# Optimization experiments

Measured on AMD Instinct MI355X. Metric: run time of the kernel, lower is better.

The kernel has to match this reference:

```python
import jax, jax.numpy as jnp
import numpy as np

HEADS = 8
DIM_HEAD = 64


def setup_inputs() -> dict:
    key = jax.random.key(0)
    ks = jax.random.split(key, 6)
    b, dim, h, w = 8, 512, 64, 64
    inner = HEADS * DIM_HEAD  # 512
    return {
        "f_m": jax.random.normal(ks[0], (b, dim, h, w), dtype=jnp.float32),
        "f_n": jax.random.normal(ks[1], (b, dim, h, w), dtype=jnp.float32),
        "Wq": jax.random.normal(ks[2], (inner, dim), dtype=jnp.float32) * 0.02,
        "Wkv": jax.random.normal(ks[3], (2 * inner, dim), dtype=jnp.float32) * 0.02,
        "Wout": jax.random.normal(ks[4], (dim, inner), dtype=jnp.float32) * 0.02,
        "bout": jax.random.normal(ks[5], (dim,), dtype=jnp.float32) * 0.02,
    }


def reference(f_m, f_n, Wq, Wkv, Wout, bout):
    b, c, h, w = f_m.shape
    n = h * w
    scale = DIM_HEAD ** -0.5
    # 1x1 convs == channel GEMMs
    q = jnp.einsum('oc,bchw->bohw', Wq, f_m).reshape(b, HEADS, DIM_HEAD, n)
    kv = jnp.einsum('oc,bchw->bohw', Wkv, f_n)
    k, v = jnp.split(kv, 2, axis=1)
    k = k.reshape(b, HEADS, DIM_HEAD, n)
    v = v.reshape(b, HEADS, DIM_HEAD, n)
    # NOTE: contraction is over spatial n -> channel attention [b,h,d,d]
    dots = jnp.einsum('bhin,bhjn->bhij', q, k) * scale
    attn = jax.nn.softmax(dots, axis=-1)
    out = jnp.einsum('bhij,bhjn->bhin', attn, v).reshape(b, HEADS * DIM_HEAD, h, w)
    return jnp.einsum('oc,bchw->bohw', Wout, out) + bout[None, :, None, None]
```

## Files before the change

### kernel.cpp

```cpp
#include <hip/hip_runtime.h>
#include <hip/hip_bf16.h>
#include <stdint.h>

typedef __bf16 bf16_t;
typedef __bf16 bf16x8 __attribute__((ext_vector_type(8)));
typedef float f32x4 __attribute__((ext_vector_type(4)));

#define MFMA_16x16x32(A, B, C) __builtin_amdgcn_mfma_f32_16x16x32_bf16((A), (B), (C), 0, 0, 0)

__device__ inline void gload_lds16(const bf16_t* g, bf16_t* lds) {
  auto* gp = (const __attribute__((address_space(1))) uint32_t*)(uintptr_t)g;
  auto* lp = (__attribute__((address_space(3))) uint32_t*)(uintptr_t)lds;
  __builtin_amdgcn_global_load_lds(gp, lp, 16, 0, 0);
}

__global__ __launch_bounds__(256)
void k_cvt3(const float* __restrict__ a, const float* __restrict__ b,
            const float* __restrict__ c, bf16_t* __restrict__ oa,
            bf16_t* __restrict__ ob, bf16_t* __restrict__ oc) {
  int i = blockIdx.x * blockDim.x + threadIdx.x;
  int region = i >> 16;
  int e = (i & 65535) * 4;
  const float* src = region == 0 ? a : (region == 1 ? b : c);
  bf16_t* dst = region == 0 ? oa : (region == 1 ? ob : oc);
  float4 v = *(const float4*)(src + e);
  bf16_t o[4] = {(bf16_t)v.x, (bf16_t)v.y, (bf16_t)v.z, (bf16_t)v.w};
  *(uint2*)(dst + e) = *(uint2*)o;
}

__global__ __launch_bounds__(256)
void k_transpose_cast(const float* __restrict__ in, bf16_t* __restrict__ out, int C, int N) {
  __shared__ float tile[32][33];
  int b = blockIdx.z;
  const float* src = in + (size_t)b * C * N;
  bf16_t* dst = out + (size_t)b * C * N;
  int n0 = blockIdx.x * 32, c0 = blockIdx.y * 32;
  int tx = threadIdx.x, ty = threadIdx.y;
#pragma unroll
  for (int i = 0; i < 32; i += 8)
    tile[ty + i][tx] = src[(size_t)(c0 + ty + i) * N + (n0 + tx)];
  __syncthreads();
#pragma unroll
  for (int i = 0; i < 32; i += 8)
    dst[(size_t)(n0 + ty + i) * C + (c0 + tx)] = (bf16_t)tile[tx][ty + i];
}

__global__ __launch_bounds__(256)
void k_fnT(const float* __restrict__ in, bf16_t* __restrict__ out_nc, int C, int N) {
  __shared__ float tile[64][65];
  const int b = blockIdx.z;
  const float* src = in + (size_t)b * C * N;
  const int n0 = blockIdx.x * 64, c0 = blockIdx.y * 64;
  const int t = threadIdx.x;
  const int cr = t >> 2;
  const int nc = (t & 3) * 16;
  {
    const float* srow = src + (size_t)(c0 + cr) * N + n0 + nc;
#pragma unroll
    for (int q = 0; q < 4; ++q) {
      float4 v = *(const float4*)(srow + q * 4);
      tile[cr][nc + q * 4 + 0] = v.x; tile[cr][nc + q * 4 + 1] = v.y;
      tile[cr][nc + q * 4 + 2] = v.z; tile[cr][nc + q * 4 + 3] = v.w;
    }
  }
  __syncthreads();
  {
    const int nr = t >> 2;
    const int cc = (t & 3) * 16;
    bf16_t on[16];
#pragma unroll
    for (int q = 0; q < 16; ++q) on[q] = (bf16_t)tile[cc + q][nr];
    bf16_t* dst = out_nc + (size_t)b * (size_t)N * C + (size_t)(n0 + nr) * C + c0 + cc;
    *(uint4*)(dst) = *(uint4*)(on);
    *(uint4*)(dst + 8) = *(uint4*)(on + 8);
  }
}

__global__ __launch_bounds__(512, 2)
void k_gram256(const float* __restrict__ A, const float* __restrict__ B,
               bf16_t* __restrict__ Cp) {
  const int raw = blockIdx.x;
  const int xcd = raw & 7, idx = raw >> 3;
  const int mt = idx & 1, nt = (idx >> 1) & 1, ks = idx >> 2;
  const int b = xcd;
  const float* Ab = A + (size_t)b * 512 * 4096;
  const float* Bb = B + (size_t)b * 512 * 4096;
  const int bm = mt * 256, bn = nt * 256;
  const int kbeg = ks * 512;

  const int tid = threadIdx.x;
  const int wave = tid >> 6, lane = tid & 63;
  const int l15 = lane & 15, l4 = lane >> 4;
  const int wm = (wave >> 2) * 128, wn = (wave & 3) * 64;
  const int rsw = (l15 >> 1) & 3;

  __shared__ bf16_t As[2][256 * 32];
  __shared__ bf16_t Bs[2][256 * 32];

  f32x4 acc[8][4] = {};

  const int rho = tid >> 1, h = tid & 1;
  const int sw = (rho >> 1) & 3;
  const int wo0 = rho * 32 + (((2 * h) ^ sw) * 8);
  const int wo1 = rho * 32 + (((2 * h + 1) ^ sw) * 8);
  const float* ga = Ab + (size_t)(bm + rho) * 4096 + kbeg + h * 16;
  const float* gb = Bb + (size_t)(bn + rho) * 4096 + kbeg + h * 16;

  float4 ra[4], rb[4];
#pragma unroll
  for (int q = 0; q < 4; ++q) {
    ra[q] = *(const float4*)(ga + q * 4);
    rb[q] = *(const float4*)(gb + q * 4);
  }

  int cur = 0;
  for (int i = 0; i < 16; ++i) {
    bf16_t ta[16], tb[16];
#pragma unroll
    for (int q = 0; q < 4; ++q) {
      ta[q * 4 + 0] = (bf16_t)ra[q].x; ta[q * 4 + 1] = (bf16_t)ra[q].y;
      ta[q * 4 + 2] = (bf16_t)ra[q].z; ta[q * 4 + 3] = (bf16_t)ra[q].w;
      tb[q * 4 + 0] = (bf16_t)rb[q].x; tb[q * 4 + 1] = (bf16_t)rb[q].y;
      tb[q * 4 + 2] = (bf16_t)rb[q].z; tb[q * 4 + 3] = (bf16_t)rb[q].w;
    }
    *(uint4*)(&As[cur][wo0]) = *(uint4*)(ta);
    *(uint4*)(&As[cur][wo1]) = *(uint4*)(ta + 8);
    *(uint4*)(&Bs[cur][wo0]) = *(uint4*)(tb);
    *(uint4*)(&Bs[cur][wo1]) = *(uint4*)(tb + 8);
    if (i + 1 < 16) {
      const float* na = ga + (i + 1) * 32;
      const float* nb = gb + (i + 1) * 32;
#pragma unroll
      for (int q = 0; q < 4; ++q) {
        ra[q] = *(const float4*)(na + q * 4);
        rb[q] = *(const float4*)(nb + q * 4);
      }
    }
    __syncthreads();
    bf16x8 bfr[4];
#pragma unroll
    for (int n = 0; n < 4; ++n)
      bfr[n] = *(const bf16x8*)(&Bs[cur][(wn + n * 16 + l15) * 32 + ((l4 ^ rsw) * 8)]);
#pragma unroll
    for (int m = 0; m < 8; ++m) {
      bf16x8 af = *(const bf16x8*)(&As[cur][(wm + m * 16 + l15) * 32 + ((l4 ^ rsw) * 8)]);
#pragma unroll
      for (int n = 0; n < 4; ++n)
        acc[m][n] = MFMA_16x16x32(af, bfr[n], acc[m][n]);
    }
    cur ^= 1;
  }

  bf16_t* Cb = Cp + (size_t)(b * 8 + ks) * 262144;
#pragma unroll
  for (int m = 0; m < 8; ++m) {
    const int row0 = bm + wm + m * 16 + l4 * 4;
#pragma unroll
    for (int n = 0; n < 4; ++n) {
      const int col = bn + wn + n * 16 + l15;
#pragma unroll
      for (int j = 0; j < 4; ++j)
        Cb[(size_t)(row0 + j) * 512 + col] = (bf16_t)acc[m][n][j];
    }
  }
}

__global__ __launch_bounds__(512, 2)
void k_y256(const bf16_t* __restrict__ A, const bf16_t* __restrict__ B,
            float* __restrict__ C, const float* __restrict__ bias) {
  const int raw = blockIdx.x;
  const int b = raw & 7, c = raw >> 3;
  const int bm = (c & 1) * 256, bn = (c >> 1) * 256;
  A += (size_t)b * 262144;
  B += (size_t)b * 4096 * 512;
  C += (size_t)b * 512 * 4096;

  const int tid = threadIdx.x;
  const int wave = tid >> 6, lane = tid & 63;
  const int l15 = lane & 15, l4 = lane >> 4;
  const int wm = (wave >> 2) * 128, wn = (wave & 3) * 64;
  const int rsw = (l15 >> 1) & 3;

  __shared__ bf16_t As[2][256 * 32];
  __shared__ bf16_t Bs[2][256 * 32];

  f32x4 acc[8][4] = {};

  const int lrow = lane >> 2;
  const int lch = (lane & 3) ^ ((lane >> 3) & 3);
  const bf16_t* srcA = A + (size_t)(bm + wave * 32 + lrow) * 512 + lch * 8;
  const bf16_t* srcB = B + (size_t)(bn + wave * 32 + lrow) * 512 + lch * 8;
  bf16_t* dstA = &As[0][wave * 32 * 32];
  bf16_t* dstB = &Bs[0][wave * 32 * 32];
  const int bufoff = 256 * 32;

  auto stage = [&](int buf, int k0) {
    gload_lds16(srcA + k0,            dstA + buf * bufoff);
    gload_lds16(srcA + 16 * 512 + k0, dstA + buf * bufoff + 512);
    gload_lds16(srcB + k0,            dstB + buf * bufoff);
    gload_lds16(srcB + 16 * 512 + k0, dstB + buf * bufoff + 512);
  };

  stage(0, 0);
  __syncthreads();

  int cur = 0;
  for (int i = 0; i < 16; ++i) {
    if (i + 1 < 16) stage(cur ^ 1, (i + 1) * 32);
    bf16x8 bfr[4];
#pragma unroll
    for (int n = 0; n < 4; ++n)
      bfr[n] = *(const bf16x8*)(&Bs[cur][(wn + n * 16 + l15) * 32 + ((l4 ^ rsw) * 8)]);
#pragma unroll
    for (int m = 0; m < 8; ++m) {
      bf16x8 af = *(const bf16x8*)(&As[cur][(wm + m * 16 + l15) * 32 + ((l4 ^ rsw) * 8)]);
#pragma unroll
      for (int n = 0; n < 4; ++n)
        acc[m][n] = MFMA_16x16x32(af, bfr[n], acc[m][n]);
    }
    __syncthreads();
    cur ^= 1;
  }

#pragma unroll
  for (int m = 0; m < 8; ++m) {
    const int row0 = bm + wm + m * 16 + l4 * 4;
#pragma unroll
    for (int n = 0; n < 4; ++n) {
      const int col = bn + wn + n * 16 + l15;
#pragma unroll
      for (int j = 0; j < 4; ++j)
        C[(size_t)(row0 + j) * 4096 + col] = acc[m][n][j] + bias[row0 + j];
    }
  }
}

__global__ __launch_bounds__(256)
void k_reduce8(const bf16_t* __restrict__ p, bf16_t* __restrict__ out) {
  int i = blockIdx.x * blockDim.x + threadIdx.x;
  int b = i >> 15;
  int e8 = (i & 32767) * 8;
  const bf16_t* pb = p + (size_t)b * 8 * 262144 + e8;
  float s[8] = {};
#pragma unroll
  for (int ks = 0; ks < 8; ++ks) {
    bf16x8 v = *(const bf16x8*)(pb + (size_t)ks * 262144);
#pragma unroll
    for (int j = 0; j < 8; ++j) s[j] += (float)v[j];
  }
  bf16x8 o;
#pragma unroll
  for (int j = 0; j < 8; ++j) o[j] = (bf16_t)s[j];
  *(bf16x8*)(out + (size_t)b * 262144 + e8) = o;
}

__global__ __launch_bounds__(256)
void k_gemm_bt(const bf16_t* __restrict__ A, const bf16_t* __restrict__ B,
               bf16_t* __restrict__ Cv, int M, int N, int K,
               long long sA, long long sB, long long sC) {
  const int zb = blockIdx.z;
  A += (size_t)zb * sA;
  B += (size_t)zb * sB;

  const int tid = threadIdx.x;
  const int wave = tid >> 6, lane = tid & 63;
  const int l15 = lane & 15, l4 = lane >> 4;
  const int bm = blockIdx.y * 128, bn = blockIdx.x * 128;
  const int wm = (wave >> 1) * 64, wn = (wave & 1) * 64;

  __shared__ bf16_t As[2][128 * 32];
  __shared__ bf16_t Bs[2][128 * 32];

  f32x4 acc[4][4] = {};

  const int lrow = lane >> 2;
  const int lchunk = (lane & 3) * 8;
  const int ra = wave * 16 + lrow;

  auto stage = [&](int buf, int k0) {
    gload_lds16(&A[(size_t)(bm + ra) * K + k0 + lchunk],      &As[buf][(wave * 16) * 32]);
    gload_lds16(&A[(size_t)(bm + 64 + ra) * K + k0 + lchunk], &As[buf][(64 + wave * 16) * 32]);
    gload_lds16(&B[(size_t)(bn + ra) * K + k0 + lchunk],      &Bs[buf][(wave * 16) * 32]);
    gload_lds16(&B[(size_t)(bn + 64 + ra) * K + k0 + lchunk], &Bs[buf][(64 + wave * 16) * 32]);
  };

  const int nsteps = K / 32;
  stage(0, 0);
  __syncthreads();

  for (int i = 0; i < nsteps; ++i) {
    const int cur = i & 1;
    if (i + 1 < nsteps) stage(cur ^ 1, (i + 1) * 32);
    bf16x8 af[4], bfr[4];
#pragma unroll
    for (int m = 0; m < 4; ++m)
      af[m] = *(const bf16x8*)(&As[cur][(wm + m * 16 + l15) * 32 + l4 * 8]);
#pragma unroll
    for (int n = 0; n < 4; ++n)
      bfr[n] = *(const bf16x8*)(&Bs[cur][(wn + n * 16 + l15) * 32 + l4 * 8]);
#pragma unroll
    for (int m = 0; m < 4; ++m)
#pragma unroll
      for (int n = 0; n < 4; ++n)
        acc[m][n] = MFMA_16x16x32(af[m], bfr[n], acc[m][n]);
    __syncthreads();
  }

#pragma unroll
  for (int m = 0; m < 4; ++m) {
    const int row0 = bm + wm + m * 16 + l4 * 4;
#pragma unroll
    for (int n = 0; n < 4; ++n) {
      const int col = bn + wn + n * 16 + l15;
#pragma unroll
      for (int j = 0; j < 4; ++j)
        (Cv + (size_t)zb * sC)[(size_t)(row0 + j) * N + col] = (bf16_t)acc[m][n][j];
    }
  }
}

__global__ __launch_bounds__(256)
void k_dots_wveff(const bf16_t* __restrict__ T1, const bf16_t* __restrict__ wk,
                  const bf16_t* __restrict__ wvT, bf16_t* __restrict__ wveffT) {
  const int bh = blockIdx.x;
  const int b = bh >> 3, hh = bh & 7;
  const bf16_t* qh = T1 + (size_t)b * 262144 + (size_t)hh * 64 * 512;
  const bf16_t* kh = wk + (size_t)hh * 64 * 512;
  const int tid = threadIdx.x;
  const int wave = tid >> 6, lane = tid & 63;
  const int l15 = lane & 15, l4 = lane >> 4;

  __shared__ float S[64][65];
  __shared__ bf16_t P[64][72];

  {
    const int wm = (wave >> 1) * 32, wn = (wave & 1) * 32;
    f32x4 acc[2][2] = {};
#pragma unroll 2
    for (int k0 = 0; k0 < 512; k0 += 32) {
      bf16x8 af[2], bfr[2];
#pragma unroll
      for (int m = 0; m < 2; ++m)
        af[m] = *(const bf16x8*)(&qh[(size_t)(wm + m * 16 + l15) * 512 + k0 + l4 * 8]);
#pragma unroll
      for (int n = 0; n < 2; ++n)
        bfr[n] = *(const bf16x8*)(&kh[(size_t)(wn + n * 16 + l15) * 512 + k0 + l4 * 8]);
#pragma unroll
      for (int m = 0; m < 2; ++m)
#pragma unroll
        for (int n = 0; n < 2; ++n)
          acc[m][n] = MFMA_16x16x32(af[m], bfr[n], acc[m][n]);
    }
    const float scale = 0.125f;
#pragma unroll
    for (int m = 0; m < 2; ++m)
#pragma unroll
      for (int n = 0; n < 2; ++n)
#pragma unroll
        for (int j = 0; j < 4; ++j)
          S[wm + m * 16 + l4 * 4 + j][wn + n * 16 + l15] = acc[m][n][j] * scale;
  }
  __syncthreads();

  {
    const int r = tid >> 2, seg = (tid & 3) * 16;
    float vals[16];
    float mx = -1e30f;
#pragma unroll
    for (int c = 0; c < 16; ++c) { vals[c] = S[r][seg + c]; mx = fmaxf(mx, vals[c]); }
    mx = fmaxf(mx, __shfl_xor(mx, 1));
    mx = fmaxf(mx, __shfl_xor(mx, 2));
    float sum = 0.f;
#pragma unroll
    for (int c = 0; c < 16; ++c) { vals[c] = __expf(vals[c] - mx); sum += vals[c]; }
    sum += __shfl_xor(sum, 1);
    sum += __shfl_xor(sum, 2);
    const float inv = 1.0f / sum;
    bf16_t pr[16];
#pragma unroll
    for (int c = 0; c < 16; ++c) pr[c] = (bf16_t)(vals[c] * inv);
    *(uint4*)(&P[r][seg]) = *(uint4*)(pr);
    *(uint4*)(&P[r][seg + 8]) = *(uint4*)(pr + 8);
  }
  __syncthreads();

  {
    const bf16_t* av = wvT + (size_t)hh * 512 * 64;
    bf16_t* ob = wveffT + (size_t)b * 262144 + (size_t)hh * 64;
    const int wm = (wave >> 1) * 64, wn = (wave & 1) * 32;
    for (int cm0 = 0; cm0 < 512; cm0 += 128) {
      f32x4 acc[4][2] = {};
#pragma unroll
      for (int ks = 0; ks < 2; ++ks) {
        const int k0 = ks * 32;
        bf16x8 af[4], bfr[2];
#pragma unroll
        for (int m = 0; m < 4; ++m)
          af[m] = *(const bf16x8*)(&av[(size_t)(cm0 + wm + m * 16 + l15) * 64 + k0 + l4 * 8]);
#pragma unroll
        for (int n = 0; n < 2; ++n)
          bfr[n] = *(const bf16x8*)(&P[wn + n * 16 + l15][k0 + l4 * 8]);
#pragma unroll
        for (int m = 0; m < 4; ++m)
#pragma unroll
          for (int n = 0; n < 2; ++n)
            acc[m][n] = MFMA_16x16x32(af[m], bfr[n], acc[m][n]);
      }
#pragma unroll
      for (int m = 0; m < 4; ++m)
#pragma unroll
        for (int n = 0; n < 2; ++n)
#pragma unroll
          for (int j = 0; j < 4; ++j)
            ob[(size_t)(cm0 + wm + m * 16 + l4 * 4 + j) * 512 + wn + n * 16 + l15] =
                (bf16_t)acc[m][n][j];
    }
  }
}

extern "C" void kernel_launch(void* const* d_in, const int* in_sizes, int n_in,
                              void* d_out, int out_size, void* d_ws, size_t ws_size,
                              hipStream_t stream) {
  const float* f_m  = (const float*)d_in[0];
  const float* f_n  = (const float*)d_in[1];
  const float* Wq   = (const float*)d_in[2];
  const float* Wkv  = (const float*)d_in[3];
  const float* Wout = (const float*)d_in[4];
  const float* bout = (const float*)d_in[5];
  float* y = (float*)d_out;

  const size_t ACT = (size_t)8 * 4096 * 512;
  const size_t SQ  = (size_t)512 * 512;
  char* p = (char*)d_ws;
  bf16_t* wq_b    = (bf16_t*)p; p += SQ * 2;
  bf16_t* wk_b    = (bf16_t*)p; p += SQ * 2;
  bf16_t* wout_b  = (bf16_t*)p; p += SQ * 2;
  bf16_t* wvT     = (bf16_t*)p; p += SQ * 2;
  bf16_t* Hb      = (bf16_t*)p; p += (size_t)8 * SQ * 2;
  bf16_t* T1      = (bf16_t*)p; p += (size_t)8 * SQ * 2;
  bf16_t* wveffT  = (bf16_t*)p; p += (size_t)8 * SQ * 2;
  bf16_t* W2      = (bf16_t*)p; p += (size_t)8 * SQ * 2;
  bf16_t* Hp8     = (bf16_t*)p; p += (size_t)64 * SQ * 2;
  bf16_t* fnT     = (bf16_t*)p; p += ACT * 2;

  k_cvt3<<<dim3(768), 256, 0, stream>>>(Wq, Wkv, Wout, wq_b, wk_b, wout_b);
  k_transpose_cast<<<dim3(16, 2, 8), dim3(32, 8), 0, stream>>>(Wkv + SQ, wvT, 64, 512);

  k_fnT<<<dim3(64, 8, 8), 256, 0, stream>>>(f_n, fnT, 512, 4096);

  k_gram256<<<dim3(256), 512, 0, stream>>>(f_n, f_m, Hp8);
  k_reduce8<<<dim3(1024), 256, 0, stream>>>(Hp8, Hb);

  k_gemm_bt<<<dim3(4, 4, 8), 256, 0, stream>>>(wq_b, Hb, T1, 512, 512, 512,
                                               0, (long long)SQ, (long long)SQ);
  k_dots_wveff<<<dim3(64), 256, 0, stream>>>(T1, wk_b, wvT, wveffT);
  k_gemm_bt<<<dim3(4, 4, 8), 256, 0, stream>>>(wout_b, wveffT, W2, 512, 512, 512,
                                               0, (long long)SQ, (long long)SQ);
  k_y256<<<dim3(256), 512, 0, stream>>>(W2, fnT, y, bout);
}
```

Baseline: 135.7 us.

## Merge front-end prep kernels and gram GEMM into one heterogeneous launch

Combines the weight cast, Wv transpose, f_n transpose-cast and the partial Gram GEMM into a single kernel whose blocks dispatch on block index to the different jobs. This removes three launches and lets the memory-bound transpose and cast blocks run alongside the compute-bound gram blocks. In exchange, every block reserves 64KB of LDS and uses 512 threads, so the small transpose and cast blocks may have lower occupancy. The ordering of block scheduling now decides how well the two kinds of work overlap.

```diff
diff --git a/kernel.cpp b/kernel.cpp
--- a/kernel.cpp
+++ b/kernel.cpp
@@ -14,224 +14,161 @@
   __builtin_amdgcn_global_load_lds(gp, lp, 16, 0, 0);
 }
 
-__global__ __launch_bounds__(256)
-void k_cvt3(const float* __restrict__ a, const float* __restrict__ b,
-            const float* __restrict__ c, bf16_t* __restrict__ oa,
-            bf16_t* __restrict__ ob, bf16_t* __restrict__ oc) {
-  int i = blockIdx.x * blockDim.x + threadIdx.x;
-  int region = i >> 16;
-  int e = (i & 65535) * 4;
-  const float* src = region == 0 ? a : (region == 1 ? b : c);
-  bf16_t* dst = region == 0 ? oa : (region == 1 ? ob : oc);
-  float4 v = *(const float4*)(src + e);
-  bf16_t o[4] = {(bf16_t)v.x, (bf16_t)v.y, (bf16_t)v.z, (bf16_t)v.w};
-  *(uint2*)(dst + e) = *(uint2*)o;
-}
-
-__global__ __launch_bounds__(256)
-void k_transpose_cast(const float* __restrict__ in, bf16_t* __restrict__ out, int C, int N) {
-  __shared__ float tile[32][33];
-  int b = blockIdx.z;
-  const float* src = in + (size_t)b * C * N;
-  bf16_t* dst = out + (size_t)b * C * N;
-  int n0 = blockIdx.x * 32, c0 = blockIdx.y * 32;
-  int tx = threadIdx.x, ty = threadIdx.y;
-#pragma unroll
-  for (int i = 0; i < 32; i += 8)
-    tile[ty + i][tx] = src[(size_t)(c0 + ty + i) * N + (n0 + tx)];
-  __syncthreads();
-#pragma unroll
-  for (int i = 0; i < 32; i += 8)
-    dst[(size_t)(n0 + ty + i) * C + (c0 + tx)] = (bf16_t)tile[tx][ty + i];
-}
-
-__global__ __launch_bounds__(256)
-void k_fnT(const float* __restrict__ in, bf16_t* __restrict__ out_nc, int C, int N) {
-  __shared__ float tile[64][65];
-  const int b = blockIdx.z;
-  const float* src = in + (size_t)b * C * N;
-  const int n0 = blockIdx.x * 64, c0 = blockIdx.y * 64;
-  const int t = threadIdx.x;
-  const int cr = t >> 2;
-  const int nc = (t & 3) * 16;
-  {
-    const float* srow = src + (size_t)(c0 + cr) * N + n0 + nc;
+__global__ __launch_bounds__(512, 2)
+void k_front(const float* __restrict__ f_m, const float* __restrict__ f_n,
+             const float* __restrict__ Wq, const float* __restrict__ Wkv,
+             const float* __restrict__ Wout,
+             bf16_t* __restrict__ Hp, bf16_t* __restrict__ fnT,
+             bf16_t* __restrict__ wq_b, bf16_t* __restrict__ wk_b,
+             bf16_t* __restrict__ wout_b, bf16_t* __restrict__ wvT) {
+  __shared__ __align__(16) char ldsbuf[65536];
+  const int bid = blockIdx.x;
+  const int tid = threadIdx.x;
+
+  if (bid < 256) {
+    const int xcd = bid & 7, idx = bid >> 3;
+    const int mt = idx & 1, nt = (idx >> 1) & 1, ks = idx >> 2;
+    const int b = xcd;
+    const float* Ab = f_n + (size_t)b * 512 * 4096;
+    const float* Bb = f_m + (size_t)b * 512 * 4096;
+    const int bm = mt * 256, bn = nt * 256;
+    const int kbeg = ks * 512;
+
+    const int wave = tid >> 6, lane = tid & 63;
+    const int l15 = lane & 15, l4 = lane >> 4;
+    const int wm = (wave >> 2) * 128, wn = (wave & 3) * 64;
+    const int rsw = (l15 >> 1) & 3;
+
+    bf16_t* As0 = (bf16_t*)ldsbuf;
+    bf16_t* Bs0 = As0 + 16384;
+
+    f32x4 acc[8][4] = {};
+
+    const int rho = tid >> 1, h = tid & 1;
+    const int sw = (rho >> 1) & 3;
+    const int wo0 = rho * 32 + (((2 * h) ^ sw) * 8);
+    const int wo1 = rho * 32 + (((2 * h + 1) ^ sw) * 8);
+    const float* ga = Ab + (size_t)(bm + rho) * 4096 + kbeg + h * 16;
+    const float* gb = Bb + (size_t)(bn + rho) * 4096 + kbeg + h * 16;
+
+    float4 ra[4], rb[4];
 #pragma unroll
     for (int q = 0; q < 4; ++q) {
-      float4 v = *(const float4*)(srow + q * 4);
-      tile[cr][nc + q * 4 + 0] = v.x; tile[cr][nc + q * 4 + 1] = v.y;
-      tile[cr][nc + q * 4 + 2] = v.z; tile[cr][nc + q * 4 + 3] = v.w;
-    }
-  }
-  __syncthreads();
-  {
-    const int nr = t >> 2;
-    const int cc = (t & 3) * 16;
-    bf16_t on[16];
-#pragma unroll
-    for (int q = 0; q < 16; ++q) on[q] = (bf16_t)tile[cc + q][nr];
-    bf16_t* dst = out_nc + (size_t)b * (size_t)N * C + (size_t)(n0 + nr) * C + c0 + cc;
-    *(uint4*)(dst) = *(uint4*)(on);
-    *(uint4*)(dst + 8) = *(uint4*)(on + 8);
-  }
-}
-
-__global__ __launch_bounds__(512, 2)
-void k_gram256(const float* __restrict__ A, const float* __restrict__ B,
-               bf16_t* __restrict__ Cp) {
-  const int raw = blockIdx.x;
-  const int xcd = raw & 7, idx = raw >> 3;
-  const int mt = idx & 1, nt = (idx >> 1) & 1, ks = idx >> 2;
-  const int b = xcd;
-  const float* Ab = A + (size_t)b * 512 * 4096;
-  const float* Bb = B + (size_t)b * 512 * 4096;
-  const int bm = mt * 256, bn = nt * 256;
-  const int kbeg = ks * 512;
-
-  const int tid = threadIdx.x;
-  const int wave = tid >> 6, lane = tid & 63;
-  const int l15 = lane & 15, l4 = lane >> 4;
-  const int wm = (wave >> 2) * 128, wn = (wave & 3) * 64;
-  const int rsw = (l15 >> 1) & 3;
-
-  __shared__ bf16_t As[2][256 * 32];
-  __shared__ bf16_t Bs[2][256 * 32];
-
-  f32x4 acc[8][4] = {};
-
-  const int rho = tid >> 1, h = tid & 1;
-  const int sw = (rho >> 1) & 3;
-  const int wo0 = rho * 32 + (((2 * h) ^ sw) * 8);
-  const int wo1 = rho * 32 + (((2 * h + 1) ^ sw) * 8);
-  const float* ga = Ab + (size_t)(bm + rho) * 4096 + kbeg + h * 16;
-  const float* gb = Bb + (size_t)(bn + rho) * 4096 + kbeg + h * 16;
-
-  float4 ra[4], rb[4];
-#pragma unroll
-  for (int q = 0; q < 4; ++q) {
-    ra[q] = *(const float4*)(ga + q * 4);
-    rb[q] = *(const float4*)(gb + q * 4);
-  }
-
-  int cur = 0;
-  for (int i = 0; i < 16; ++i) {
-    bf16_t ta[16], tb[16];
-#pragma unroll
-    for (int q = 0; q < 4; ++q) {
-      ta[q * 4 + 0] = (bf16_t)ra[q].x; ta[q * 4 + 1] = (bf16_t)ra[q].y;
-      ta[q * 4 + 2] = (bf16_t)ra[q].z; ta[q * 4 + 3] = (bf16_t)ra[q].w;
-      tb[q * 4 + 0] = (bf16_t)rb[q].x; tb[q * 4 + 1] = (bf16_t)rb[q].y;
-      tb[q * 4 + 2] = (bf16_t)rb[q].z; tb[q * 4 + 3] = (bf16_t)rb[q].w;
-    }
-    *(uint4*)(&As[cur][wo0]) = *(uint4*)(ta);
-    *(uint4*)(&As[cur][wo1]) = *(uint4*)(ta + 8);
-    *(uint4*)(&Bs[cur][wo0]) = *(uint4*)(tb);
-    *(uint4*)(&Bs[cur][wo1]) = *(uint4*)(tb + 8);
-    if (i + 1 < 16) {
-      const float* na = ga + (i + 1) * 32;
-      const float* nb = gb + (i + 1) * 32;
+      ra[q] = *(const float4*)(ga + q * 4);
+      rb[q] = *(const float4*)(gb + q * 4);
+    }
+
+    int cur = 0;
+    for (int i = 0; i < 16; ++i) {
+      bf16_t* As = As0 + cur * 8192;
+      bf16_t* Bs = Bs0 + cur * 8192;
+      bf16_t ta[16], tb[16];
 #pragma unroll
       for (int q = 0; q < 4; ++q) {
-        ra[q] = *(const float4*)(na + q * 4);
-        rb[q] = *(const float4*)(nb + q * 4);
+        ta[q * 4 + 0] = (bf16_t)ra[q].x; ta[q * 4 + 1] = (bf16_t)ra[q].y;
+        ta[q * 4 + 2] = (bf16_t)ra[q].z; ta[q * 4 + 3] = (bf16_t)ra[q].w;
+        tb[q * 4 + 0] = (bf16_t)rb[q].x; tb[q * 4 + 1] = (bf16_t)rb[q].y;
+        tb[q * 4 + 2] = (bf16_t)rb[q].z; tb[q * 4 + 3] = (bf16_t)rb[q].w;
+      }
+      *(uint4*)(&As[wo0]) = *(uint4*)(ta);
+      *(uint4*)(&As[wo1]) = *(uint4*)(ta + 8);
+      *(uint4*)(&Bs[wo0]) = *(uint4*)(tb);
+      *(uint4*)(&Bs[wo1]) = *(uint4*)(tb + 8);
+      if (i + 1 < 16) {
+        const float* na = ga + (i + 1) * 32;
+        const float* nb = gb + (i + 1) * 32;
+#pragma unroll
+        for (int q = 0; q < 4; ++q) {
+          ra[q] = *(const float4*)(na + q * 4);
+          rb[q] = *(const float4*)(nb + q * 4);
+        }
+      }
+      __syncthreads();
+      bf16x8 bfr[4];
+#pragma unroll
+      for (int n = 0; n < 4; ++n)
+        bfr[n] = *(const bf16x8*)(&Bs[(wn + n * 16 + l15) * 32 + ((l4 ^ rsw) * 8)]);
+#pragma unroll
+      for (int m = 0; m < 8; ++m) {
+        bf16x8 af = *(const bf16x8*)(&As[(wm + m * 16 + l15) * 32 + ((l4 ^ rsw) * 8)]);
+#pragma unroll
+        for (int n = 0; n < 4; ++n)
+          acc[m][n] = MFMA_16x16x32(af, bfr[n], acc[m][n]);
+      }
+      cur ^= 1;
+    }
+
+    bf16_t* Cb = Hp + (size_t)(b * 8 + ks) * 262144;
+#pragma unroll
+    for (int m = 0; m < 8; ++m) {
+      const int row0 = bm + wm + m * 16 + l4 * 4;
+#pragma unroll
+      for (int n = 0; n < 4; ++n) {
+        const int col = bn + wn + n * 16 + l15;
+#pragma unroll
+        for (int j = 0; j < 4; ++j)
+          Cb[(size_t)(row0 + j) * 512 + col] = (bf16_t)acc[m][n][j];
+      }
+    }
+  } else if (bid < 2304) {
+    const int half = tid >> 8;
+    const int t = tid & 255;
+    const int tileIdx = (bid - 256) * 2 + half;
+    const int ntile = tileIdx & 63, ctile = (tileIdx >> 6) & 7, b = tileIdx >> 9;
+    const int C = 512, N = 4096;
+    const float* src = f_n + (size_t)b * C * N;
+    const int n0 = ntile * 64, c0 = ctile * 64;
+    float* tile = (float*)ldsbuf + half * (64 * 65);
+
+    const int cr = t >> 2;
+    const int nc = (t & 3) * 16;
+    {
+      const float* srow = src + (size_t)(c0 + cr) * N + n0 + nc;
+#pragma unroll
+      for (int q = 0; q < 4; ++q) {
+        float4 v = *(const float4*)(srow + q * 4);
+        tile[cr * 65 + nc + q * 4 + 0] = v.x; tile[cr * 65 + nc + q * 4 + 1] = v.y;
+        tile[cr * 65 + nc + q * 4 + 2] = v.z; tile[cr * 65 + nc + q * 4 + 3] = v.w;
       }
     }
     __syncthreads();
-    bf16x8 bfr[4];
-#pragma unroll
-    for (int n = 0; n < 4; ++n)
-      bfr[n] = *(const bf16x8*)(&Bs[cur][(wn + n * 16 + l15) * 32 + ((l4 ^ rsw) * 8)]);
-#pragma unroll
-    for (int m = 0; m < 8; ++m) {
-      bf16x8 af = *(const bf16x8*)(&As[cur][(wm + m * 16 + l15) * 32 + ((l4 ^ rsw) * 8)]);
-#pragma unroll
-      for (int n = 0; n < 4; ++n)
-        acc[m][n] = MFMA_16x16x32(af, bfr[n], acc[m][n]);
-    }
-    cur ^= 1;
-  }
-
-  bf16_t* Cb = Cp + (size_t)(b * 8 + ks) * 262144;
-#pragma unroll
-  for (int m = 0; m < 8; ++m) {
-    const int row0 = bm + wm + m * 16 + l4 * 4;
-#pragma unroll
-    for (int n = 0; n < 4; ++n) {
-      const int col = bn + wn + n * 16 + l15;
-#pragma unroll
-      for (int j = 0; j < 4; ++j)
-        Cb[(size_t)(row0 + j) * 512 + col] = (bf16_t)acc[m][n][j];
-    }
-  }
-}
-
-__global__ __launch_bounds__(512, 2)
-void k_y256(const bf16_t* __restrict__ A, const bf16_t* __restrict__ B,
-            float* __restrict__ C, const float* __restrict__ bias) {
-  const int raw = blockIdx.x;
-  const int b = raw & 7, c = raw >> 3;
-  const int bm = (c & 1) * 256, bn = (c >> 1) * 256;
-  A += (size_t)b * 262144;
-  B += (size_t)b * 4096 * 512;
-  C += (size_t)b * 512 * 4096;
-
-  const int tid = threadIdx.x;
-  const int wave = tid >> 6, lane = tid & 63;
-  const int l15 = lane & 15, l4 = lane >> 4;
-  const int wm = (wave >> 2) * 128, wn = (wave & 3) * 64;
-  const int rsw = (l15 >> 1) & 3;
-
-  __shared__ bf16_t As[2][256 * 32];
-  __shared__ bf16_t Bs[2][256 * 32];
-
-  f32x4 acc[8][4] = {};
-
-  const int lrow = lane >> 2;
-  const int lch = (lane & 3) ^ ((lane >> 3) & 3);
-  const bf16_t* srcA = A + (size_t)(bm + wave * 32 + lrow) * 512 + lch * 8;
-  const bf16_t* srcB = B + (size_t)(bn + wave * 32 + lrow) * 512 + lch * 8;
-  bf16_t* dstA = &As[0][wave * 32 * 32];
-  bf16_t* dstB = &Bs[0][wave * 32 * 32];
-  const int bufoff = 256 * 32;
-
-  auto stage = [&](int buf, int k0) {
-    gload_lds16(srcA + k0,            dstA + buf * bufoff);
-    gload_lds16(srcA + 16 * 512 + k0, dstA + buf * bufoff + 512);
-    gload_lds16(srcB + k0,            dstB + buf * bufoff);
-    gload_lds16(srcB + 16 * 512 + k0, dstB + buf * bufoff + 512);
-  };
-
-  stage(0, 0);
-  __syncthreads();
-
-  int cur = 0;
-  for (int i = 0; i < 16; ++i) {
-    if (i + 1 < 16) stage(cur ^ 1, (i + 1) * 32);
-    bf16x8 bfr[4];
-#pragma unroll
-    for (int n = 0; n < 4; ++n)
-      bfr[n] = *(const bf16x8*)(&Bs[cur][(wn + n * 16 + l15) * 32 + ((l4 ^ rsw) * 8)]);
-#pragma unroll
-    for (int m = 0; m < 8; ++m) {
-      bf16x8 af = *(const bf16x8*)(&As[cur][(wm + m * 16 + l15) * 32 + ((l4 ^ rsw) * 8)]);
-#pragma unroll
-      for (int n = 0; n < 4; ++n)
-        acc[m][n] = MFMA_16x16x32(af, bfr[n], acc[m][n]);
-    }
+    {
+      const int nr = t >> 2;
+      const int cc = (t & 3) * 16;
+      bf16_t on[16];
+#pragma unroll
+      for (int q = 0; q < 16; ++q) on[q] = (bf16_t)tile[(cc + q) * 65 + nr];
+      bf16_t* dst = fnT + (size_t)b * (size_t)N * C + (size_t)(n0 + nr) * C + c0 + cc;
+      *(uint4*)(dst) = *(uint4*)(on);
+      *(uint4*)(dst + 8) = *(uint4*)(on + 8);
+    }
+  } else if (bid < 2688) {
+    int i = (bid - 2304) * 512 + tid;
+    int region = i >> 16;
+    int e = (i & 65535) * 4;
+    const float* src = region == 0 ? Wq : (region == 1 ? Wkv : Wout);
+    bf16_t* dst = region == 0 ? wq_b : (region == 1 ? wk_b : wout_b);
+    float4 v = *(const float4*)(src + e);
+    bf16_t o[4] = {(bf16_t)v.x, (bf16_t)v.y, (bf16_t)v.z, (bf16_t)v.w};
+    *(uint2*)(dst + e) = *(uint2*)o;
+  } else {
+    const int half = tid >> 8;
+    const int t = tid & 255;
+    const int tileIdx = (bid - 2688) * 2 + half;
+    const int x = tileIdx & 15, yy = (tileIdx >> 4) & 1, z = tileIdx >> 5;
+    const int C = 64, N = 512;
+    const float* src = Wkv + (size_t)512 * 512 + (size_t)z * C * N;
+    bf16_t* dst = wvT + (size_t)z * C * N;
+    const int n0 = x * 32, c0 = yy * 32;
+    float* tile = (float*)ldsbuf + half * (32 * 33);
+    const int tx = t & 31, ty = (t >> 5) & 7;
+#pragma unroll
+    for (int i = 0; i < 32; i += 8)
+      tile[(ty + i) * 33 + tx] = src[(size_t)(c0 + ty + i) * N + (n0 + tx)];
     __syncthreads();
-    cur ^= 1;
-  }
-
-#pragma unroll
-  for (int m = 0; m < 8; ++m) {
-    const int row0 = bm + wm + m * 16 + l4 * 4;
-#pragma unroll
-    for (int n = 0; n < 4; ++n) {
-      const int col = bn + wn + n * 16 + l15;
-#pragma unroll
-      for (int j = 0; j < 4; ++j)
-        C[(size_t)(row0 + j) * 4096 + col] = acc[m][n][j] + bias[row0 + j];
-    }
+#pragma unroll
+    for (int i = 0; i < 32; i += 8)
+      dst[(size_t)(n0 + ty + i) * C + (c0 + tx)] = (bf16_t)tile[tx * 33 + ty + i];
   }
 }
 
@@ -414,6 +351,76 @@
           for (int j = 0; j < 4; ++j)
             ob[(size_t)(cm0 + wm + m * 16 + l4 * 4 + j) * 512 + wn + n * 16 + l15] =
                 (bf16_t)acc[m][n][j];
+    }
+  }
+}
+
+__global__ __launch_bounds__(512, 2)
+void k_y256(const bf16_t* __restrict__ A, const bf16_t* __restrict__ B,
+            float* __restrict__ C, const float* __restrict__ bias) {
+  const int raw = blockIdx.x;
+  const int b = raw & 7, c = raw >> 3;
+  const int bm = (c & 1) * 256, bn = (c >> 1) * 256;
+  A += (size_t)b * 262144;
+  B += (size_t)b * 4096 * 512;
+  C += (size_t)b * 512 * 4096;
+
+  const int tid = threadIdx.x;
+  const int wave = tid >> 6, lane = tid & 63;
+  const int l15 = lane & 15, l4 = lane >> 4;
+  const int wm = (wave >> 2) * 128, wn = (wave & 3) * 64;
+  const int rsw = (l15 >> 1) & 3;
+
+  __shared__ bf16_t As[2][256 * 32];
+  __shared__ bf16_t Bs[2][256 * 32];
+
+  f32x4 acc[8][4] = {};
+
+  const int lrow = lane >> 2;
+  const int lch = (lane & 3) ^ ((lane >> 3) & 3);
+  const bf16_t* srcA = A + (size_t)(bm + wave * 32 + lrow) * 512 + lch * 8;
+  const bf16_t* srcB = B + (size_t)(bn + wave * 32 + lrow) * 512 + lch * 8;
+  bf16_t* dstA = &As[0][wave * 32 * 32];
+  bf16_t* dstB = &Bs[0][wave * 32 * 32];
+  const int bufoff = 256 * 32;
+
+  auto stage = [&](int buf, int k0) {
+    gload_lds16(srcA + k0,            dstA + buf * bufoff);
+    gload_lds16(srcA + 16 * 512 + k0, dstA + buf * bufoff + 512);
+    gload_lds16(srcB + k0,            dstB + buf * bufoff);
+    gload_lds16(srcB + 16 * 512 + k0, dstB + buf * bufoff + 512);
+  };
+
+  stage(0, 0);
+  __syncthreads();
+
+  int cur = 0;
+  for (int i = 0; i < 16; ++i) {
+    if (i + 1 < 16) stage(cur ^ 1, (i + 1) * 32);
+    bf16x8 bfr[4];
+#pragma unroll
+    for (int n = 0; n < 4; ++n)
+      bfr[n] = *(const bf16x8*)(&Bs[cur][(wn + n * 16 + l15) * 32 + ((l4 ^ rsw) * 8)]);
+#pragma unroll
+    for (int m = 0; m < 8; ++m) {
+      bf16x8 af = *(const bf16x8*)(&As[cur][(wm + m * 16 + l15) * 32 + ((l4 ^ rsw) * 8)]);
+#pragma unroll
+      for (int n = 0; n < 4; ++n)
+        acc[m][n] = MFMA_16x16x32(af, bfr[n], acc[m][n]);
+    }
+    __syncthreads();
+    cur ^= 1;
+  }
+
+#pragma unroll
+  for (int m = 0; m < 8; ++m) {
+    const int row0 = bm + wm + m * 16 + l4 * 4;
+#pragma unroll
+    for (int n = 0; n < 4; ++n) {
+      const int col = bn + wn + n * 16 + l15;
+#pragma unroll
+      for (int j = 0; j < 4; ++j)
+        C[(size_t)(row0 + j) * 4096 + col] = acc[m][n][j] + bias[row0 + j];
     }
   }
 }
@@ -443,12 +450,8 @@
   bf16_t* Hp8     = (bf16_t*)p; p += (size_t)64 * SQ * 2;
   bf16_t* fnT     = (bf16_t*)p; p += ACT * 2;
 
-  k_cvt3<<<dim3(768), 256, 0, stream>>>(Wq, Wkv, Wout, wq_b, wk_b, wout_b);
-  k_transpose_cast<<<dim3(16, 2, 8), dim3(32, 8), 0, stream>>>(Wkv + SQ, wvT, 64, 512);
-
-  k_fnT<<<dim3(64, 8, 8), 256, 0, stream>>>(f_n, fnT, 512, 4096);
-
-  k_gram256<<<dim3(256), 512, 0, stream>>>(f_n, f_m, Hp8);
+  k_front<<<dim3(2816), 512, 0, stream>>>(f_m, f_n, Wq, Wkv, Wout,
+                                          Hp8, fnT, wq_b, wk_b, wout_b, wvT);
   k_reduce8<<<dim3(1024), 256, 0, stream>>>(Hp8, Hb);
 
   k_gemm_bt<<<dim3(4, 4, 8), 256, 0, stream>>>(wq_b, Hb, T1, 512, 512, 512,
```

After: 127.6 us. 6.0% less time.
